# Kernel optimization log

Measured on AMD Instinct MI355X. Metric: run time of the kernel, lower is better.

The kernel has to match this reference:

```python
import jax, jax.numpy as jnp
import numpy as np

SOFTCAP = 30.0  # final_logit_softcapping (Gemma2)


def setup_inputs() -> dict:
    key = jax.random.key(0)
    ks = jax.random.split(key, 6)
    B, S, D, V = 32, 8, 2048, 128000
    return {
        "embedding": jax.random.normal(ks[0], (V, D), jnp.float32) * 0.02,
        "hidden_states": jax.random.normal(ks[1], (B, S, D), jnp.float32),
        "temperatures": jax.random.uniform(ks[2], (B,), jnp.float32, 0.5, 1.0),
        "top_ps": jax.random.uniform(ks[3], (B,), jnp.float32, 0.5, 1.0),
        "output_positions": jax.random.randint(ks[4], (1,), 0, S),
        "top_ks": jax.random.randint(ks[5], (B,), 1, 64),
    }


def reference(embedding, hidden_states, temperatures, top_ps, output_positions, top_ks):
    # select decode position: [B, 1, D] -> [B, D]
    hs = jnp.take(hidden_states, output_positions, axis=1).squeeze(1)
    # logits over vocab: [B, V]
    logits = jnp.einsum("bd,vd->bv", hs, embedding)
    # final logit softcapping
    logits = jnp.tanh(logits / SOFTCAP) * SOFTCAP
    # temperature scaling (matches in-place div; returned logits are scaled)
    logits = logits / temperatures[:, None]
    probs = jax.nn.softmax(logits.astype(jnp.float32), axis=-1)
    # sort descending
    idx = jnp.argsort(-probs, axis=-1)                      # [B, V]
    probs_sort = jnp.take_along_axis(probs, idx, axis=-1)   # [B, V]
    cum = jnp.cumsum(probs_sort, axis=-1)
    V = probs.shape[-1]
    mask = ((cum - probs_sort) > top_ps[:, None]) | (
        jnp.arange(V)[None, :] >= top_ks[:, None]
    )
    probs_sort = jnp.where(mask, 0.0, probs_sort)
    probs_sort = probs_sort / probs_sort.sum(axis=-1, keepdims=True)
    # scatter back to vocab order
    inv = jnp.argsort(idx, axis=-1)
    probs_final = jnp.take_along_axis(probs_sort, inv, axis=-1)
    # multinomial sample (one draw per row)
    next_token_ids = jax.random.categorical(
        jax.random.key(42), jnp.log(probs_final), axis=-1
    )
    return next_token_ids, logits
```

## Files before the change

### kernel.cpp

```cpp
#include <hip/hip_runtime.h>
#include <float.h>
#include <math.h>

#define VOCAB 128000
#define DIM   2048
#define SEQL  8
#define NB    32
#define SCAP  4096

__device__ __forceinline__ unsigned f2sortable(float x){
  unsigned u = __float_as_uint(x);
  return (u & 0x80000000u) ? ~u : (u | 0x80000000u);
}
__device__ __forceinline__ float inv_sortable(unsigned u){
  unsigned v = (u & 0x80000000u) ? (u ^ 0x80000000u) : ~u;
  return __uint_as_float(v);
}
__device__ __forceinline__ unsigned rotl32(unsigned x, int d){
  return (x << d) | (x >> (32 - d));
}

__device__ float jax_gumbel(unsigned n){
  unsigned x0 = 0u, x1 = n;
  const unsigned k0 = 0u, k1 = 42u;
  const unsigned k2 = 0x1BD11BDAu ^ k0 ^ k1;
  x0 += k0; x1 += k1;
#define TFR(r) { x0 += x1; x1 = rotl32(x1, r); x1 ^= x0; }
  TFR(13) TFR(15) TFR(26) TFR(6)
  x0 += k1; x1 += k2 + 1u;
  TFR(17) TFR(29) TFR(16) TFR(24)
  x0 += k2; x1 += k0 + 2u;
  TFR(13) TFR(15) TFR(26) TFR(6)
  x0 += k0; x1 += k1 + 3u;
  TFR(17) TFR(29) TFR(16) TFR(24)
  x0 += k1; x1 += k2 + 4u;
  TFR(13) TFR(15) TFR(26) TFR(6)
  x0 += k2; x1 += k0 + 5u;
#undef TFR
  unsigned bits = x0 ^ x1;
  float f = __uint_as_float((bits >> 9) | 0x3f800000u) - 1.0f;
  float u = f + 1.17549435e-38f;
  return -logf(-logf(u));
}

__global__ __launch_bounds__(256) void k_logits(
    const float* __restrict__ E, const float* __restrict__ HS,
    const float* __restrict__ temps, const int* __restrict__ posp,
    float* __restrict__ C, unsigned* __restrict__ rowmax_u)
{
  __shared__ float tile[NB * 32];
  const int tid  = threadIdx.x;
  const int w    = tid >> 6;
  const int lane = tid & 63;
  const int g    = lane >> 4;
  const int qi   = lane & 15;
  const int pos  = posp[0];
  const int vbase = blockIdx.x * 32;
  const int vw    = vbase + w * 8;

  float acc[8][8];
#pragma unroll
  for (int j = 0; j < 8; ++j)
#pragma unroll
    for (int bl = 0; bl < 8; ++bl) acc[j][bl] = 0.f;

  const float* Eb = E + (size_t)vw * DIM + (qi << 2);
  const float* Hb = HS + ((size_t)((g * 8) * SEQL + pos)) * DIM + (qi << 2);

  for (int s = 0; s < 32; ++s){
    const float* Ebs = Eb + s * 64;
    const float* Hbs = Hb + s * 64;
    float4 e[8];
#pragma unroll
    for (int j = 0; j < 8; ++j)
      e[j] = *(const float4*)(Ebs + (size_t)j * DIM);
#pragma unroll
    for (int bl = 0; bl < 8; ++bl){
      float4 h = *(const float4*)(Hbs + (size_t)bl * (SEQL * DIM));
#pragma unroll
      for (int j = 0; j < 8; ++j){
        acc[j][bl] = fmaf(e[j].x, h.x, acc[j][bl]);
        acc[j][bl] = fmaf(e[j].y, h.y, acc[j][bl]);
        acc[j][bl] = fmaf(e[j].z, h.z, acc[j][bl]);
        acc[j][bl] = fmaf(e[j].w, h.w, acc[j][bl]);
      }
    }
  }

#pragma unroll
  for (int j = 0; j < 8; ++j)
#pragma unroll
    for (int bl = 0; bl < 8; ++bl){
      float v = acc[j][bl];
      v += __shfl_xor(v, 1, 64);
      v += __shfl_xor(v, 2, 64);
      v += __shfl_xor(v, 4, 64);
      v += __shfl_xor(v, 8, 64);
      acc[j][bl] = v;
    }
  if (qi == 0){
#pragma unroll
    for (int j = 0; j < 8; ++j)
#pragma unroll
      for (int bl = 0; bl < 8; ++bl)
        tile[(g * 8 + bl) * 32 + w * 8 + j] = acc[j][bl];
  }
  __syncthreads();
  {
    const int b = tid >> 3, vq = tid & 7;
    const float tmp = temps[b];
    float4 tv = *(const float4*)&tile[b * 32 + vq * 4];
    float4 o;
    o.x = (tanhf(tv.x / 30.f) * 30.f) / tmp;
    o.y = (tanhf(tv.y / 30.f) * 30.f) / tmp;
    o.z = (tanhf(tv.z / 30.f) * 30.f) / tmp;
    o.w = (tanhf(tv.w / 30.f) * 30.f) / tmp;
    *(float4*)(C + (size_t)b * VOCAB + vbase + vq * 4) = o;
    float m4 = fmaxf(fmaxf(o.x, o.y), fmaxf(o.z, o.w));
    m4 = fmaxf(m4, __shfl_xor(m4, 1, 64));
    m4 = fmaxf(m4, __shfl_xor(m4, 2, 64));
    m4 = fmaxf(m4, __shfl_xor(m4, 4, 64));
    if (vq == 0) atomicMax(&rowmax_u[b], f2sortable(m4));
  }
}

__global__ __launch_bounds__(1024) void k_sample_fused(
    const float* __restrict__ C,
    const float* __restrict__ tps, const int* __restrict__ tks,
    const unsigned* __restrict__ rowmax_u, float* __restrict__ out_tok)
{
  const int b = blockIdx.x, t = threadIdx.x;
  const float* row = C + (size_t)b * VOCAB;
  __shared__ float red[1024];
  __shared__ unsigned ps[1024];
  __shared__ unsigned hist[4096];
  __shared__ float    cval_s[SCAP];
  __shared__ int      cidx_s[SCAP];
  __shared__ int tbin_s;
  __shared__ unsigned cnt_s;

  if (t == 0) cnt_s = 0u;
  const float m = inv_sortable(rowmax_u[b]);
  for (int i = t; i < 4096; i += 1024) hist[i] = 0u;
  __syncthreads();

  float zs = 0.f;
  for (int f = t; f < VOCAB / 4; f += 1024){
    float4 x4 = ((const float4*)row)[f];
    float xs[4] = {x4.x, x4.y, x4.z, x4.w};
#pragma unroll
    for (int c = 0; c < 4; ++c){
      zs += expf(xs[c] - m);
      atomicAdd(&hist[f2sortable(xs[c]) >> 20], 1u);
    }
  }
  red[t] = zs; __syncthreads();
  for (int sft = 512; sft > 0; sft >>= 1){
    if (t < sft) red[t] += red[t + sft];
    __syncthreads();
  }
  const float Z = red[0];

  unsigned s_t = 0u;
#pragma unroll
  for (int k = 0; k < 4; ++k) s_t += hist[t * 4 + k];
  ps[t] = s_t; __syncthreads();
  for (int off = 1; off < 1024; off <<= 1){
    unsigned v = ps[t] + ((t + off < 1024) ? ps[t + off] : 0u);
    __syncthreads();
    ps[t] = v;
    __syncthreads();
  }
  const unsigned Sstrict = ps[t] - s_t;
  if (Sstrict < 64u && ps[t] >= 64u){
    unsigned c = Sstrict;
    for (int bb = 3; bb >= 0; --bb){
      c += hist[t * 4 + bb];
      if (c >= 64u){ tbin_s = t * 4 + bb; break; }
    }
  }
  __syncthreads();
  const unsigned thr = ((unsigned)tbin_s) << 20;

  for (int f = t; f < VOCAB / 4; f += 1024){
    float4 x4 = ((const float4*)row)[f];
    float xs[4] = {x4.x, x4.y, x4.z, x4.w};
#pragma unroll
    for (int c = 0; c < 4; ++c){
      if (f2sortable(xs[c]) >= thr){
        unsigned slot = atomicAdd(&cnt_s, 1u);
        if (slot < (unsigned)SCAP){
          cval_s[slot] = xs[c];
          cidx_s[slot] = f * 4 + c;
        }
      }
    }
  }
  __syncthreads();
  int cn = (int)cnt_s; if (cn > SCAP) cn = SCAP;

  for (int j = t; j < cn; j += 1024)
    cval_s[j] = expf(cval_s[j] - m) / Z;
  __syncthreads();

  if (t < 64){
    float my_sp = 0.f; int my_si = 0;
    float lp = FLT_MAX; int li = -1;
    for (int r = 0; r < 64; ++r){
      float bp = -1.f; int bi = 0x7fffffff;
      for (int j = t; j < cn; j += 64){
        float p = cval_s[j]; int id = cidx_s[j];
        bool valid = (p < lp) || (p == lp && id > li);
        if (valid && (p > bp || (p == bp && id < bi))){ bp = p; bi = id; }
      }
#pragma unroll
      for (int off = 32; off >= 1; off >>= 1){
        float op = __shfl_xor(bp, off, 64);
        int   oi = __shfl_xor(bi, off, 64);
        if (op > bp || (op == bp && oi < bi)){ bp = op; bi = oi; }
      }
      if (t == r){ my_sp = bp; my_si = bi; }
      lp = bp; li = bi;
    }

    const float tp = tps[b];
    const int   tk = tks[b];
    float c = 0.f, sren = 0.f;
    bool keep_me = false;
    for (int j = 0; j < 64; ++j){
      float pj = __shfl(my_sp, j, 64);
      c = c + pj;
      float excl = c - pj;
      bool keep = (!(excl > tp)) && (j < tk);
      if (j == t) keep_me = keep;
      if (keep) sren = sren + pj;
    }

    float score = -FLT_MAX;
    int vid = my_si;
    if (keep_me){
      float pf = my_sp / sren;
      score = logf(pf) + jax_gumbel((unsigned)(b * VOCAB + vid));
    }
    float bs = score; int bv = vid;
#pragma unroll
    for (int off = 32; off >= 1; off >>= 1){
      float os = __shfl_xor(bs, off, 64);
      int   ov = __shfl_xor(bv, off, 64);
      if (os > bs || (os == bs && ov < bv)){ bs = os; bv = ov; }
    }
    if (t == 0) out_tok[b] = (float)bv;
  }
}

extern "C" void kernel_launch(void* const* d_in, const int* in_sizes, int n_in,
                              void* d_out, int out_size, void* d_ws, size_t ws_size,
                              hipStream_t stream)
{
  (void)in_sizes; (void)n_in; (void)out_size; (void)ws_size;
  const float* emb   = (const float*)d_in[0];
  const float* hs    = (const float*)d_in[1];
  const float* temps = (const float*)d_in[2];
  const float* tps   = (const float*)d_in[3];
  const int*   posp  = (const int*)d_in[4];
  const int*   tks   = (const int*)d_in[5];
  float* out = (float*)d_out;
  float* C   = out + NB;

  unsigned* rowmax_u = (unsigned*)d_ws;
  hipMemsetAsync(rowmax_u, 0, NB * sizeof(unsigned), stream);

  k_logits      <<<dim3(VOCAB / 32), dim3(256),  0, stream>>>(emb, hs, temps, posp, C, rowmax_u);
  k_sample_fused<<<dim3(NB),         dim3(1024), 0, stream>>>(C, tps, tks, rowmax_u, out);
}
```

Measured before the change: 521.1 us.

## Remap logits GEMV so each block covers 8 vocab rows across all batches

The logits kernel now assigns 8 vocab rows per block, with each wave handling 8 batch rows and all 64 lanes splitting the full K dimension. This replaces the shared-memory tile and __syncthreads. The embedding tile is now read by all four waves of a block, relying on cache hits, and the grid is four times larger. The epilogue writes scalar, strided outputs instead of float4 rows, which may hurt store coalescing, and issues more atomicMax operations.

```diff
diff --git a/kernel.cpp b/kernel.cpp
--- a/kernel.cpp
+++ b/kernel.cpp
@@ -48,15 +48,11 @@
     const float* __restrict__ temps, const int* __restrict__ posp,
     float* __restrict__ C, unsigned* __restrict__ rowmax_u)
 {
-  __shared__ float tile[NB * 32];
   const int tid  = threadIdx.x;
   const int w    = tid >> 6;
   const int lane = tid & 63;
-  const int g    = lane >> 4;
-  const int qi   = lane & 15;
   const int pos  = posp[0];
-  const int vbase = blockIdx.x * 32;
-  const int vw    = vbase + w * 8;
+  const int vb   = blockIdx.x * 8;
 
   float acc[8][8];
 #pragma unroll
@@ -64,27 +60,29 @@
 #pragma unroll
     for (int bl = 0; bl < 8; ++bl) acc[j][bl] = 0.f;
 
-  const float* Eb = E + (size_t)vw * DIM + (qi << 2);
-  const float* Hb = HS + ((size_t)((g * 8) * SEQL + pos)) * DIM + (qi << 2);
-
-  for (int s = 0; s < 32; ++s){
-    const float* Ebs = Eb + s * 64;
-    const float* Hbs = Hb + s * 64;
-    float4 e[8];
+  const float* Eb = E + (size_t)vb * DIM + (lane << 2);
+  const float* Hb = HS + ((size_t)(w * 8 * SEQL + pos)) * DIM + (lane << 2);
+
+#pragma unroll 1
+  for (int s = 0; s < 8; ++s){
+    const float* Ebs = Eb + s * 256;
+    const float* Hbs = Hb + s * 256;
+    float4 e[8], h[8];
 #pragma unroll
     for (int j = 0; j < 8; ++j)
       e[j] = *(const float4*)(Ebs + (size_t)j * DIM);
 #pragma unroll
-    for (int bl = 0; bl < 8; ++bl){
-      float4 h = *(const float4*)(Hbs + (size_t)bl * (SEQL * DIM));
-#pragma unroll
-      for (int j = 0; j < 8; ++j){
-        acc[j][bl] = fmaf(e[j].x, h.x, acc[j][bl]);
-        acc[j][bl] = fmaf(e[j].y, h.y, acc[j][bl]);
-        acc[j][bl] = fmaf(e[j].z, h.z, acc[j][bl]);
-        acc[j][bl] = fmaf(e[j].w, h.w, acc[j][bl]);
-      }
-    }
+    for (int bl = 0; bl < 8; ++bl)
+      h[bl] = *(const float4*)(Hbs + (size_t)bl * (SEQL * DIM));
+#pragma unroll
+    for (int j = 0; j < 8; ++j)
+#pragma unroll
+      for (int bl = 0; bl < 8; ++bl){
+        acc[j][bl] = fmaf(e[j].x, h[bl].x, acc[j][bl]);
+        acc[j][bl] = fmaf(e[j].y, h[bl].y, acc[j][bl]);
+        acc[j][bl] = fmaf(e[j].z, h[bl].z, acc[j][bl]);
+        acc[j][bl] = fmaf(e[j].w, h[bl].w, acc[j][bl]);
+      }
   }
 
 #pragma unroll
@@ -96,32 +94,29 @@
       v += __shfl_xor(v, 2, 64);
       v += __shfl_xor(v, 4, 64);
       v += __shfl_xor(v, 8, 64);
+      v += __shfl_xor(v, 16, 64);
+      v += __shfl_xor(v, 32, 64);
       acc[j][bl] = v;
     }
-  if (qi == 0){
-#pragma unroll
-    for (int j = 0; j < 8; ++j)
-#pragma unroll
-      for (int bl = 0; bl < 8; ++bl)
-        tile[(g * 8 + bl) * 32 + w * 8 + j] = acc[j][bl];
-  }
-  __syncthreads();
-  {
-    const int b = tid >> 3, vq = tid & 7;
-    const float tmp = temps[b];
-    float4 tv = *(const float4*)&tile[b * 32 + vq * 4];
-    float4 o;
-    o.x = (tanhf(tv.x / 30.f) * 30.f) / tmp;
-    o.y = (tanhf(tv.y / 30.f) * 30.f) / tmp;
-    o.z = (tanhf(tv.z / 30.f) * 30.f) / tmp;
-    o.w = (tanhf(tv.w / 30.f) * 30.f) / tmp;
-    *(float4*)(C + (size_t)b * VOCAB + vbase + vq * 4) = o;
-    float m4 = fmaxf(fmaxf(o.x, o.y), fmaxf(o.z, o.w));
-    m4 = fmaxf(m4, __shfl_xor(m4, 1, 64));
-    m4 = fmaxf(m4, __shfl_xor(m4, 2, 64));
-    m4 = fmaxf(m4, __shfl_xor(m4, 4, 64));
-    if (vq == 0) atomicMax(&rowmax_u[b], f2sortable(m4));
-  }
+
+  float val = 0.f;
+#pragma unroll
+  for (int j = 0; j < 8; ++j)
+#pragma unroll
+    for (int bl = 0; bl < 8; ++bl)
+      if (lane == j * 8 + bl) val = acc[j][bl];
+
+  const int jj = lane >> 3;
+  const int bb = lane & 7;
+  const int b  = w * 8 + bb;
+  const float o = (tanhf(val / 30.f) * 30.f) / temps[b];
+  C[(size_t)b * VOCAB + vb + jj] = o;
+
+  float m8 = o;
+  m8 = fmaxf(m8, __shfl_xor(m8, 8, 64));
+  m8 = fmaxf(m8, __shfl_xor(m8, 16, 64));
+  m8 = fmaxf(m8, __shfl_xor(m8, 32, 64));
+  if (jj == 0) atomicMax(&rowmax_u[b], f2sortable(m8));
 }
 
 __global__ __launch_bounds__(1024) void k_sample_fused(
@@ -270,6 +265,6 @@
   unsigned* rowmax_u = (unsigned*)d_ws;
   hipMemsetAsync(rowmax_u, 0, NB * sizeof(unsigned), stream);
 
-  k_logits      <<<dim3(VOCAB / 32), dim3(256),  0, stream>>>(emb, hs, temps, posp, C, rowmax_u);
-  k_sample_fused<<<dim3(NB),         dim3(1024), 0, stream>>>(C, tps, tks, rowmax_u, out);
-}
+  k_logits      <<<dim3(VOCAB / 8), dim3(256),  0, stream>>>(emb, hs, temps, posp, C, rowmax_u);
+  k_sample_fused<<<dim3(NB),        dim3(1024), 0, stream>>>(C, tps, tks, rowmax_u, out);
+}
```

After: 608.5 us. +16.8%, slower.
